# Kernel optimization log

Hardware: AMD Instinct MI355X
Metric: run time of the kernel (lower is better)

The kernel has to match this reference:

```python
import jax, jax.numpy as jnp
import numpy as np
import math

N_HEAD = 16

def _rope(x):
    # x: [B, H, T, D], D even; interleaved-pair rotation as in the torch code
    B, H, T, D = x.shape
    theta = 10000.0 ** (-2.0 * jnp.arange(D // 2, dtype=x.dtype) / D)  # [D/2]
    pos = jnp.arange(T, dtype=x.dtype)[:, None]                        # [T,1]
    ang = pos * theta[None, :]                                          # [T, D/2]
    sin, cos = jnp.sin(ang), jnp.cos(ang)
    x1, x2 = x[..., ::2], x[..., 1::2]
    x1r = x1 * cos - x2 * sin
    x2r = x1 * sin + x2 * cos
    # re-interleave
    out = jnp.stack([x1r, x2r], axis=-1).reshape(B, H, T, D)
    return out

def setup_inputs() -> dict:
    key = jax.random.key(0)
    ks = jax.random.split(key, 3)
    B, T, C = 4, 2048, 1024
    x = jax.random.normal(ks[0], (B, T, C), dtype=jnp.float32)
    W_qkv = jax.random.normal(ks[1], (C, 3 * C), dtype=jnp.float32) * (1.0 / math.sqrt(C))
    b_qkv = jnp.zeros((3 * C,), dtype=jnp.float32)
    W_proj = jax.random.normal(ks[2], (C, C), dtype=jnp.float32) * (1.0 / math.sqrt(C))
    b_proj = jnp.zeros((C,), dtype=jnp.float32)
    return {"x": x, "W_qkv": W_qkv, "b_qkv": b_qkv, "W_proj": W_proj, "b_proj": b_proj}

def reference(x, W_qkv, b_qkv, W_proj, b_proj):
    B, T, C = x.shape
    H = N_HEAD
    D = C // H
    qkv = x @ W_qkv + b_qkv                      # [B,T,3C]
    q, k, v = jnp.split(qkv, 3, axis=-1)
    def to_heads(t):
        return t.reshape(B, T, H, D).transpose(0, 2, 1, 3)  # [B,H,T,D]
    q, k, v = to_heads(q), to_heads(k), to_heads(v)
    q = _rope(q)
    k = _rope(k)
    att = jnp.einsum('bhqd,bhkd->bhqk', q, k) * (1.0 / math.sqrt(D))
    mask = jnp.tril(jnp.ones((T, T), dtype=bool))
    att = jnp.where(mask[None, None, :, :], att, -jnp.inf)
    att = jax.nn.softmax(att, axis=-1)
    y = jnp.einsum('bhqk,bhkd->bhqd', att, v)    # [B,H,T,D]
    y = y.transpose(0, 2, 1, 3).reshape(B, T, C)
    return y @ W_proj + b_proj
```

## Files before the change

kernel.cpp:

```cpp
#include <hip/hip_runtime.h>
#include <cstddef>

#define B_DIM 4
#define T_DIM 2048
#define C_DIM 1024
#define H_DIM 16
#define D_DIM 64
#define C3_DIM 3072

typedef __attribute__((ext_vector_type(8))) __bf16 bf16x8;
typedef __attribute__((ext_vector_type(4))) __bf16 bf16x4;
typedef __attribute__((ext_vector_type(2))) __bf16 bf16x2;
typedef __attribute__((ext_vector_type(4))) float f32x4;

typedef const __attribute__((address_space(1))) unsigned int* gptr_t;
typedef __attribute__((address_space(3))) unsigned int* lptr_t;

__global__ __launch_bounds__(256) void cvt_bf16(const float* __restrict__ in,
                                                __bf16* __restrict__ out)
{
    int i = (blockIdx.x * 256 + threadIdx.x) * 4;
    float4 v = *(const float4*)&in[i];
    bf16x4 o = { (__bf16)v.x, (__bf16)v.y, (__bf16)v.z, (__bf16)v.w };
    *(bf16x4*)&out[i] = o;
}

__global__ __launch_bounds__(256) void transpose_cvt(
    const float* __restrict__ W, __bf16* __restrict__ Wt, int K, int N)
{
    __shared__ float tile[64][65];
    const int tid = threadIdx.x;
    const int n0 = blockIdx.x * 64, k0 = blockIdx.y * 64;
    const int tx = tid & 15, ty = tid >> 4;
#pragma unroll
    for (int it = 0; it < 4; ++it) {
        int r = it * 16 + ty;
        *(float4*)&tile[r][tx * 4] =
            *(const float4*)&W[(size_t)(k0 + r) * N + n0 + tx * 4];
    }
    __syncthreads();
    int c = tid >> 2, t0 = (tid & 3) * 16;
    __align__(16) __bf16 tmp[16];
#pragma unroll
    for (int j = 0; j < 16; ++j) tmp[j] = (__bf16)tile[t0 + j][c];
    __bf16* o = Wt + (size_t)(n0 + c) * K + k0 + t0;
    *(bf16x8*)o = *(bf16x8*)&tmp[0];
    *(bf16x8*)(o + 8) = *(bf16x8*)&tmp[8];
}

template <bool OUT_BF16>
__global__ __launch_bounds__(256) void gemm_bt(
    const __bf16* __restrict__ A, const __bf16* __restrict__ Bt,
    const float* __restrict__ bias, void* __restrict__ Cout,
    int M, int N, int K)
{
    __shared__ __align__(16) __bf16 Af[8][64][8];
    __shared__ __align__(16) __bf16 Bf[8][64][8];
    const int tid = threadIdx.x;
    const int lane = tid & 63, w = tid >> 6;
    const int lm = lane & 15, lq = lane >> 4;
    const int wm = w >> 1, wn = w & 1;
    const int m0 = blockIdx.y * 128, n0 = blockIdx.x * 128;

    const __bf16* a0 = A + (size_t)(m0 + w * 32 + lm) * K + lq * 8;
    const __bf16* a1 = a0 + (size_t)16 * K;
    const __bf16* b0 = Bt + (size_t)(n0 + w * 32 + lm) * K + lq * 8;
    const __bf16* b1 = b0 + (size_t)16 * K;

    f32x4 acc[4][4];
#pragma unroll
    for (int i = 0; i < 4; ++i)
#pragma unroll
        for (int j = 0; j < 4; ++j) acc[i][j] = (f32x4){0.f, 0.f, 0.f, 0.f};

    for (int k0 = 0; k0 < K; k0 += 32) {
        __syncthreads();
        __builtin_amdgcn_global_load_lds((gptr_t)(const void*)(a0 + k0),
                                         (lptr_t)(void*)&Af[w * 2 + 0][0][0], 16, 0, 0);
        __builtin_amdgcn_global_load_lds((gptr_t)(const void*)(a1 + k0),
                                         (lptr_t)(void*)&Af[w * 2 + 1][0][0], 16, 0, 0);
        __builtin_amdgcn_global_load_lds((gptr_t)(const void*)(b0 + k0),
                                         (lptr_t)(void*)&Bf[w * 2 + 0][0][0], 16, 0, 0);
        __builtin_amdgcn_global_load_lds((gptr_t)(const void*)(b1 + k0),
                                         (lptr_t)(void*)&Bf[w * 2 + 1][0][0], 16, 0, 0);
        __syncthreads();

        bf16x8 av[4], bv[4];
#pragma unroll
        for (int i = 0; i < 4; ++i) {
            av[i] = *(const bf16x8*)&Af[wm * 4 + i][lane][0];
            bv[i] = *(const bf16x8*)&Bf[wn * 4 + i][lane][0];
        }
#pragma unroll
        for (int i = 0; i < 4; ++i)
#pragma unroll
            for (int j = 0; j < 4; ++j)
                acc[i][j] = __builtin_amdgcn_mfma_f32_16x16x32_bf16(
                    av[i], bv[j], acc[i][j], 0, 0, 0);
    }

#pragma unroll
    for (int i = 0; i < 4; ++i) {
        int rowb = m0 + wm * 64 + i * 16 + lq * 4;
#pragma unroll
        for (int j = 0; j < 4; ++j) {
            int col = n0 + wn * 64 + j * 16 + lm;
            float bcol = bias[col];
#pragma unroll
            for (int r = 0; r < 4; ++r) {
                float v = acc[i][j][r] + bcol;
                if (OUT_BF16)
                    ((__bf16*)Cout)[(size_t)(rowb + r) * N + col] = (__bf16)v;
                else
                    ((float*)Cout)[(size_t)(rowb + r) * N + col] = v;
            }
        }
    }
}

__global__ __launch_bounds__(256) void ropecvt(
    __bf16* qkv, __bf16* __restrict__ Kb, __bf16* __restrict__ Vt)
{
    __shared__ __bf16 vt[64][72];
    const int tid = threadIdx.x;
    const int t0 = blockIdx.x * 64;
    const int bh = blockIdx.y;
    const int b = bh >> 4, h = bh & 15;
    __bf16* base = qkv + ((size_t)(b * T_DIM + t0)) * C3_DIM + h * D_DIM;

    {
        int rr = tid >> 3, cc = (tid & 7) * 8;
#pragma unroll
        for (int it = 0; it < 2; ++it) {
            int r = it * 32 + rr;
            *(bf16x8*)&vt[r][cc] =
                *(const bf16x8*)&base[(size_t)r * C3_DIM + 2 * C_DIM + cc];
        }
    }

    const float QSCALE = 0.125f * 1.44269504089f;

#pragma unroll
    for (int p = 0; p < 8; ++p) {
        int idx = tid + p * 256;
        int tl = idx >> 5, i = idx & 31;
        float theta = powf(10000.0f, -(float)i / 32.0f);
        float ang = (float)(t0 + tl) * theta;
        float s, c;
        sincosf(ang, &s, &c);
        __bf16* qp = &base[(size_t)tl * C3_DIM + 2 * i];
        float qx = (float)qp[0], qy = (float)qp[1];
        bf16x2 qo = { (__bf16)((qx * c - qy * s) * QSCALE),
                      (__bf16)((qx * s + qy * c) * QSCALE) };
        *(bf16x2*)qp = qo;
        float kx = (float)qp[C_DIM], ky = (float)qp[C_DIM + 1];
        bf16x2 ko = { (__bf16)(kx * c - ky * s), (__bf16)(kx * s + ky * c) };
        *(bf16x2*)(Kb + ((size_t)bh * T_DIM + t0 + tl) * D_DIM + 2 * i) = ko;
    }

    __syncthreads();

    int dd = tid >> 2, tc0 = (tid & 3) * 16;
    __align__(16) __bf16 tmp[16];
#pragma unroll
    for (int j = 0; j < 16; ++j) tmp[j] = vt[tc0 + j][dd];
    __bf16* vo = Vt + ((size_t)bh * D_DIM + dd) * T_DIM + t0 + tc0;
    *(bf16x8*)vo = *(bf16x8*)&tmp[0];
    *(bf16x8*)(vo + 8) = *(bf16x8*)&tmp[8];
}

__global__ __launch_bounds__(256) void attn_mfma(
    const __bf16* __restrict__ qkvb, const __bf16* __restrict__ Kb,
    const __bf16* __restrict__ Vt, __bf16* __restrict__ yb)
{
    __shared__ __align__(16) __bf16 Kf[8][64][8];
    __shared__ __align__(16) __bf16 Vf[8][64][8];
    __shared__ __align__(16) __bf16 Pb[4][16][72];

    const int tid = threadIdx.x;
    const int bh = blockIdx.x;
    const int qt = 31 - blockIdx.y;
    const int b = bh >> 4, h = bh & 15;
    const int lane = tid & 63, w = tid >> 6;
    const int m = lane & 15, qq = lane >> 4;

    const __bf16* qrow = qkvb +
        ((size_t)(b * T_DIM + qt * 64 + w * 16 + m)) * C3_DIM + h * D_DIM + qq * 8;
    bf16x8 qreg[2];
    qreg[0] = *(const bf16x8*)qrow;
    qreg[1] = *(const bf16x8*)(qrow + 32);

    float m_i = -1e30f, l_i = 0.f;
    f32x4 acc[4];
#pragma unroll
    for (int db = 0; db < 4; ++db) acc[db] = (f32x4){0.f, 0.f, 0.f, 0.f};

    const __bf16* kgbase = Kb + (size_t)bh * T_DIM * D_DIM;
    const __bf16* vgbase = Vt + (size_t)bh * D_DIM * T_DIM;

    for (int kt = 0; kt <= qt; ++kt) {
        __syncthreads();
#pragma unroll
        for (int c = 0; c < 2; ++c) {
            const __bf16* kg = kgbase +
                ((size_t)(kt * 64 + w * 16 + m)) * D_DIM + c * 32 + qq * 8;
            __builtin_amdgcn_global_load_lds(
                (gptr_t)(const void*)kg,
                (lptr_t)(void*)&Kf[w * 2 + c][0][0], 16, 0, 0);
            const __bf16* vg = vgbase +
                ((size_t)(w * 16 + m)) * T_DIM + kt * 64 + c * 32 + qq * 8;
            __builtin_amdgcn_global_load_lds(
                (gptr_t)(const void*)vg,
                (lptr_t)(void*)&Vf[w * 2 + c][0][0], 16, 0, 0);
        }
        __syncthreads();

        f32x4 sv[4];
#pragma unroll
        for (int nb = 0; nb < 4; ++nb) {
            f32x4 s = (f32x4){0.f, 0.f, 0.f, 0.f};
            s = __builtin_amdgcn_mfma_f32_16x16x32_bf16(
                *(const bf16x8*)&Kf[nb * 2 + 0][lane][0], qreg[0], s, 0, 0, 0);
            s = __builtin_amdgcn_mfma_f32_16x16x32_bf16(
                *(const bf16x8*)&Kf[nb * 2 + 1][lane][0], qreg[1], s, 0, 0, 0);
            sv[nb] = s;
        }

        if (kt == qt) {
            int qlocal = w * 16 + m;
#pragma unroll
            for (int nb = 0; nb < 4; ++nb) {
                int tb = nb * 16 + qq * 4;
#pragma unroll
                for (int r = 0; r < 4; ++r)
                    if (tb + r > qlocal) sv[nb][r] = -1e30f;
            }
        }

        float mt0 = fmaxf(fmaxf(sv[0][0], sv[0][1]), fmaxf(sv[0][2], sv[0][3]));
        float mt1 = fmaxf(fmaxf(sv[1][0], sv[1][1]), fmaxf(sv[1][2], sv[1][3]));
        float mt2 = fmaxf(fmaxf(sv[2][0], sv[2][1]), fmaxf(sv[2][2], sv[2][3]));
        float mt3 = fmaxf(fmaxf(sv[3][0], sv[3][1]), fmaxf(sv[3][2], sv[3][3]));
        float mt = fmaxf(fmaxf(mt0, mt1), fmaxf(mt2, mt3));
        mt = fmaxf(mt, __shfl_xor(mt, 16));
        mt = fmaxf(mt, __shfl_xor(mt, 32));
        float mnew = fmaxf(m_i, mt);
        float alpha = exp2f(m_i - mnew);
        float ll = 0.f;
#pragma unroll
        for (int nb = 0; nb < 4; ++nb) {
            float p0 = exp2f(sv[nb][0] - mnew);
            float p1 = exp2f(sv[nb][1] - mnew);
            float p2 = exp2f(sv[nb][2] - mnew);
            float p3 = exp2f(sv[nb][3] - mnew);
            sv[nb][0] = p0; sv[nb][1] = p1; sv[nb][2] = p2; sv[nb][3] = p3;
            ll += (p0 + p1) + (p2 + p3);
        }
        ll += __shfl_xor(ll, 16);
        ll += __shfl_xor(ll, 32);
        l_i = l_i * alpha + ll;
        m_i = mnew;
#pragma unroll
        for (int db = 0; db < 4; ++db) {
            acc[db][0] *= alpha; acc[db][1] *= alpha;
            acc[db][2] *= alpha; acc[db][3] *= alpha;
        }

#pragma unroll
        for (int nb = 0; nb < 4; ++nb) {
            bf16x4 pv = { (__bf16)sv[nb][0], (__bf16)sv[nb][1],
                          (__bf16)sv[nb][2], (__bf16)sv[nb][3] };
            *(bf16x4*)&Pb[w][m][nb * 16 + qq * 4] = pv;
        }

        bf16x8 pf0 = *(const bf16x8*)&Pb[w][m][0 * 32 + qq * 8];
        bf16x8 pf1 = *(const bf16x8*)&Pb[w][m][1 * 32 + qq * 8];

#pragma unroll
        for (int db = 0; db < 4; ++db) {
            acc[db] = __builtin_amdgcn_mfma_f32_16x16x32_bf16(
                *(const bf16x8*)&Vf[db * 2 + 0][lane][0], pf0, acc[db], 0, 0, 0);
            acc[db] = __builtin_amdgcn_mfma_f32_16x16x32_bf16(
                *(const bf16x8*)&Vf[db * 2 + 1][lane][0], pf1, acc[db], 0, 0, 0);
        }
    }

    float inv = 1.0f / l_i;
    __bf16* yrow = yb + (size_t)(b * T_DIM + qt * 64 + w * 16 + m) * C_DIM +
                   h * D_DIM + qq * 4;
#pragma unroll
    for (int db = 0; db < 4; ++db) {
        bf16x4 o = { (__bf16)(acc[db][0] * inv), (__bf16)(acc[db][1] * inv),
                     (__bf16)(acc[db][2] * inv), (__bf16)(acc[db][3] * inv) };
        *(bf16x4*)(yrow + db * 16) = o;
    }
}

extern "C" void kernel_launch(void* const* d_in, const int* in_sizes, int n_in,
                              void* d_out, int out_size, void* d_ws, size_t ws_size,
                              hipStream_t stream)
{
    const float* x     = (const float*)d_in[0];
    const float* Wqkv  = (const float*)d_in[1];
    const float* bqkv  = (const float*)d_in[2];
    const float* Wproj = (const float*)d_in[3];
    const float* bproj = (const float*)d_in[4];
    float* out = (float*)d_out;

    char* ws = (char*)d_ws;
    __bf16* qkvb = (__bf16*)(ws);
    __bf16* xb   = (__bf16*)(ws + 50331648ull);
    __bf16* yb   = (__bf16*)(ws + 67108864ull);
    __bf16* Kb   = (__bf16*)(ws + 83886080ull);
    __bf16* Vt   = (__bf16*)(ws + 100663296ull);
    __bf16* Wqt  = (__bf16*)(ws + 117440512ull);
    __bf16* Wpt  = (__bf16*)(ws + 123731968ull);

    dim3 blk(256);

    cvt_bf16<<<dim3((B_DIM * T_DIM * C_DIM) / 1024), blk, 0, stream>>>(x, xb);
    transpose_cvt<<<dim3(C3_DIM / 64, C_DIM / 64), blk, 0, stream>>>(
        Wqkv, Wqt, C_DIM, C3_DIM);
    transpose_cvt<<<dim3(C_DIM / 64, C_DIM / 64), blk, 0, stream>>>(
        Wproj, Wpt, C_DIM, C_DIM);

    gemm_bt<true><<<dim3(C3_DIM / 128, (B_DIM * T_DIM) / 128), blk, 0, stream>>>(
        xb, Wqt, bqkv, qkvb, B_DIM * T_DIM, C3_DIM, C_DIM);

    ropecvt<<<dim3(T_DIM / 64, B_DIM * H_DIM), blk, 0, stream>>>(qkvb, Kb, Vt);

    attn_mfma<<<dim3(B_DIM * H_DIM, T_DIM / 64), blk, 0, stream>>>(
        qkvb, Kb, Vt, yb);

    gemm_bt<false><<<dim3(C_DIM / 128, (B_DIM * T_DIM) / 128), blk, 0, stream>>>(
        yb, Wpt, bproj, out, B_DIM * T_DIM, C_DIM, C_DIM);
}
```

Before: 341.5 us.

## Register-prefetch next tiles in GEMM and attention, vectorize GEMM epilogue, fast RoPE trig

```diff
diff --git a/kernel.cpp b/kernel.cpp
--- a/kernel.cpp
+++ b/kernel.cpp
@@ -12,9 +12,6 @@
 typedef __attribute__((ext_vector_type(4))) __bf16 bf16x4;
 typedef __attribute__((ext_vector_type(2))) __bf16 bf16x2;
 typedef __attribute__((ext_vector_type(4))) float f32x4;
-
-typedef const __attribute__((address_space(1))) unsigned int* gptr_t;
-typedef __attribute__((address_space(3))) unsigned int* lptr_t;
 
 __global__ __launch_bounds__(256) void cvt_bf16(const float* __restrict__ in,
                                                 __bf16* __restrict__ out)
@@ -73,17 +70,24 @@
 #pragma unroll
         for (int j = 0; j < 4; ++j) acc[i][j] = (f32x4){0.f, 0.f, 0.f, 0.f};
 
+    bf16x8 ra0 = *(const bf16x8*)a0;
+    bf16x8 ra1 = *(const bf16x8*)a1;
+    bf16x8 rb0 = *(const bf16x8*)b0;
+    bf16x8 rb1 = *(const bf16x8*)b1;
+
     for (int k0 = 0; k0 < K; k0 += 32) {
         __syncthreads();
-        __builtin_amdgcn_global_load_lds((gptr_t)(const void*)(a0 + k0),
-                                         (lptr_t)(void*)&Af[w * 2 + 0][0][0], 16, 0, 0);
-        __builtin_amdgcn_global_load_lds((gptr_t)(const void*)(a1 + k0),
-                                         (lptr_t)(void*)&Af[w * 2 + 1][0][0], 16, 0, 0);
-        __builtin_amdgcn_global_load_lds((gptr_t)(const void*)(b0 + k0),
-                                         (lptr_t)(void*)&Bf[w * 2 + 0][0][0], 16, 0, 0);
-        __builtin_amdgcn_global_load_lds((gptr_t)(const void*)(b1 + k0),
-                                         (lptr_t)(void*)&Bf[w * 2 + 1][0][0], 16, 0, 0);
+        *(bf16x8*)&Af[w * 2 + 0][lane][0] = ra0;
+        *(bf16x8*)&Af[w * 2 + 1][lane][0] = ra1;
+        *(bf16x8*)&Bf[w * 2 + 0][lane][0] = rb0;
+        *(bf16x8*)&Bf[w * 2 + 1][lane][0] = rb1;
         __syncthreads();
+
+        int kn = (k0 + 32 < K) ? k0 + 32 : 0;
+        ra0 = *(const bf16x8*)(a0 + kn);
+        ra1 = *(const bf16x8*)(a1 + kn);
+        rb0 = *(const bf16x8*)(b0 + kn);
+        rb1 = *(const bf16x8*)(b1 + kn);
 
         bf16x8 av[4], bv[4];
 #pragma unroll
@@ -96,23 +100,26 @@
 #pragma unroll
             for (int j = 0; j < 4; ++j)
                 acc[i][j] = __builtin_amdgcn_mfma_f32_16x16x32_bf16(
-                    av[i], bv[j], acc[i][j], 0, 0, 0);
+                    bv[j], av[i], acc[i][j], 0, 0, 0);
     }
 
 #pragma unroll
     for (int i = 0; i < 4; ++i) {
-        int rowb = m0 + wm * 64 + i * 16 + lq * 4;
+        size_t row = (size_t)(m0 + wm * 64 + i * 16 + lm);
 #pragma unroll
         for (int j = 0; j < 4; ++j) {
-            int col = n0 + wn * 64 + j * 16 + lm;
-            float bcol = bias[col];
-#pragma unroll
-            for (int r = 0; r < 4; ++r) {
-                float v = acc[i][j][r] + bcol;
-                if (OUT_BF16)
-                    ((__bf16*)Cout)[(size_t)(rowb + r) * N + col] = (__bf16)v;
-                else
-                    ((float*)Cout)[(size_t)(rowb + r) * N + col] = v;
+            int col = n0 + wn * 64 + j * 16 + lq * 4;
+            float4 b4 = *(const float4*)&bias[col];
+            float v0 = acc[i][j][0] + b4.x;
+            float v1 = acc[i][j][1] + b4.y;
+            float v2 = acc[i][j][2] + b4.z;
+            float v3 = acc[i][j][3] + b4.w;
+            if (OUT_BF16) {
+                bf16x4 o = { (__bf16)v0, (__bf16)v1, (__bf16)v2, (__bf16)v3 };
+                *(bf16x4*)&((__bf16*)Cout)[row * N + col] = o;
+            } else {
+                float4 o = make_float4(v0, v1, v2, v3);
+                *(float4*)&((float*)Cout)[row * N + col] = o;
             }
         }
     }
@@ -144,10 +151,10 @@
     for (int p = 0; p < 8; ++p) {
         int idx = tid + p * 256;
         int tl = idx >> 5, i = idx & 31;
-        float theta = powf(10000.0f, -(float)i / 32.0f);
+        float theta = exp2f(-0.41524101186f * (float)i);
         float ang = (float)(t0 + tl) * theta;
         float s, c;
-        sincosf(ang, &s, &c);
+        __sincosf(ang, &s, &c);
         __bf16* qp = &base[(size_t)tl * C3_DIM + 2 * i];
         float qx = (float)qp[0], qy = (float)qp[1];
         bf16x2 qo = { (__bf16)((qx * c - qy * s) * QSCALE),
@@ -195,25 +202,29 @@
 #pragma unroll
     for (int db = 0; db < 4; ++db) acc[db] = (f32x4){0.f, 0.f, 0.f, 0.f};
 
-    const __bf16* kgbase = Kb + (size_t)bh * T_DIM * D_DIM;
-    const __bf16* vgbase = Vt + (size_t)bh * D_DIM * T_DIM;
+    const __bf16* kg0 = Kb + (size_t)bh * T_DIM * D_DIM +
+                        (size_t)(w * 16 + m) * D_DIM + qq * 8;
+    const __bf16* vg0 = Vt + (size_t)bh * D_DIM * T_DIM +
+                        (size_t)(w * 16 + m) * T_DIM + qq * 8;
+
+    bf16x8 kr0 = *(const bf16x8*)(kg0);
+    bf16x8 kr1 = *(const bf16x8*)(kg0 + 32);
+    bf16x8 vr0 = *(const bf16x8*)(vg0);
+    bf16x8 vr1 = *(const bf16x8*)(vg0 + 32);
 
     for (int kt = 0; kt <= qt; ++kt) {
         __syncthreads();
-#pragma unroll
-        for (int c = 0; c < 2; ++c) {
-            const __bf16* kg = kgbase +
-                ((size_t)(kt * 64 + w * 16 + m)) * D_DIM + c * 32 + qq * 8;
-            __builtin_amdgcn_global_load_lds(
-                (gptr_t)(const void*)kg,
-                (lptr_t)(void*)&Kf[w * 2 + c][0][0], 16, 0, 0);
-            const __bf16* vg = vgbase +
-                ((size_t)(w * 16 + m)) * T_DIM + kt * 64 + c * 32 + qq * 8;
-            __builtin_amdgcn_global_load_lds(
-                (gptr_t)(const void*)vg,
-                (lptr_t)(void*)&Vf[w * 2 + c][0][0], 16, 0, 0);
-        }
+        *(bf16x8*)&Kf[w * 2 + 0][lane][0] = kr0;
+        *(bf16x8*)&Kf[w * 2 + 1][lane][0] = kr1;
+        *(bf16x8*)&Vf[w * 2 + 0][lane][0] = vr0;
+        *(bf16x8*)&Vf[w * 2 + 1][lane][0] = vr1;
         __syncthreads();
+
+        int ktn = (kt < qt) ? kt + 1 : kt;
+        kr0 = *(const bf16x8*)(kg0 + (size_t)ktn * 64 * D_DIM);
+        kr1 = *(const bf16x8*)(kg0 + (size_t)ktn * 64 * D_DIM + 32);
+        vr0 = *(const bf16x8*)(vg0 + ktn * 64);
+        vr1 = *(const bf16x8*)(vg0 + ktn * 64 + 32);
 
         f32x4 sv[4];
 #pragma unroll
```

After: 342.8 us. About the same (+0.4%).
